# Kernel tuning notes

Measured on AMD Instinct MI355X. Metric: run time of the kernel, lower is better.

Reference implementation:

```python
import jax, jax.numpy as jnp
import numpy as np

N = 50000      # nodes
E = 800000     # edges
D = 128        # h_dim
R = 8          # num_rel
B = 4          # num_bases (< R -> basis decomposition)
L = 2          # num_conv
BN_EPS = 1e-3  # keras BatchNormalization default epsilon


def setup_inputs() -> dict:
    key = jax.random.key(0)
    ks = jax.random.split(key, 10)
    node_feat = jax.random.normal(ks[0], (N, D), dtype=jnp.float32)
    src = jax.random.randint(ks[1], (E,), 0, N)
    dst = jax.random.randint(ks[2], (E,), 0, N)
    etype = jax.random.randint(ks[3], (E,), 0, R)
    s = 1.0 / np.sqrt(D)
    W_emb = jax.random.normal(ks[4], (D, D), dtype=jnp.float32) * s
    b_emb = jnp.zeros((D,), dtype=jnp.float32)
    bases = jax.random.normal(ks[5], (L, B, D, D), dtype=jnp.float32) * s
    w_coe = jax.random.normal(ks[6], (L, R, B), dtype=jnp.float32) * 0.3
    self_loop = jax.random.normal(ks[7], (L, D, D), dtype=jnp.float32) * s
    bn_gamma = jnp.ones((L, D), dtype=jnp.float32)
    bn_beta = jnp.zeros((L, D), dtype=jnp.float32)
    bn_mean = jnp.zeros((L, D), dtype=jnp.float32)
    bn_var = jnp.ones((L, D), dtype=jnp.float32)
    return {"node_feat": node_feat, "W_emb": W_emb, "b_emb": b_emb,
            "bases": bases, "w_coe": w_coe, "self_loop": self_loop,
            "bn_gamma": bn_gamma, "bn_beta": bn_beta,
            "bn_mean": bn_mean, "bn_var": bn_var,
            "src": src, "dst": dst, "etype": etype}


def _edge_norm(etype, dst, dtype):
    # compute_norm: per edge type r, node_norm[dst] = 1/(#edges of type r into dst),
    # later types overwrite earlier ones (tensor_scatter_nd_update in the loop).
    node_norm = jnp.zeros((N,), dtype=dtype)
    for r in range(R):  # unique edge types, fixed ascending order
        mask = (etype == r).astype(dtype)
        cnt = jax.ops.segment_sum(mask, dst, num_segments=N)
        node_norm = jnp.where(cnt > 0, 1.0 / jnp.maximum(cnt, 1.0), node_norm)
    return node_norm[dst][:, None]  # [E, 1], norm of each edge's destination


def reference(node_feat, W_emb, b_emb, bases, w_coe, self_loop,
              bn_gamma, bn_beta, bn_mean, bn_var, src, dst, etype):
    # embedding Dense
    h = node_feat @ W_emb + b_emb                     # [N, D]
    norm = _edge_norm(etype, dst, h.dtype)            # [E, 1]
    for l in range(L):
        # basis decomposition: W[r] = sum_b w_coe[r,b] * bases[b]
        W = jnp.einsum('rb,bdf->rdf', w_coe[l], bases[l])   # [R, D, D]
        # transform all nodes under every relation, then gather per edge
        # (same math as per-type boolean_mask + matmul in low_mem path)
        T = jnp.einsum('nd,rdf->rnf', h, W)                 # [R, N, D]
        msg = T[etype, src] * norm                          # [E, D]
        agg = jax.ops.segment_sum(msg, dst, num_segments=N) # sum reduce -> [N, D]
        h = agg + h @ self_loop[l]
        # BatchNormalization, inference mode (training=None)
        h = bn_gamma[l] * (h - bn_mean[l]) * jax.lax.rsqrt(bn_var[l] + BN_EPS) + bn_beta[l]
        h = jax.nn.relu(h)
        # Dropout is identity at inference
    return h
```

## Files before the change

### kernel.cpp

```cpp
#include <hip/hip_runtime.h>

#define Dh 128
#define NN 50000
#define EE 800000
#define RR 8
#define BB 4
#define LL 2
#define KTOT 640
#define KA0 512
#define BN_EPS 1e-3f
#define NR (NN * RR)
#define NBLK 196

#define N8    (NN * Dh / 8)
#define BT_N  (LL * Dh * KTOT)
#define WE_N  (Dh * Dh)
#define EPI_N (3 * Dh)
#define Z4_N  (NR / 4)
#define PREP_TOT (N8 + BT_N + WE_N + EPI_N + Z4_N)

typedef __attribute__((ext_vector_type(8))) short bf16x8;
typedef __attribute__((ext_vector_type(4))) float f32x4;

__device__ inline unsigned short f2bf(float x) {
    unsigned u = __float_as_uint(x);
    unsigned r = (u + 0x7fffu + ((u >> 16) & 1u)) >> 16;
    return (unsigned short)r;
}

__global__ __launch_bounds__(256) void prep_kernel(
    const float* __restrict__ nf, const float* __restrict__ bases,
    const float* __restrict__ self_loop, const float* __restrict__ W_emb,
    const float* __restrict__ b_emb,
    const float* __restrict__ bn_gamma, const float* __restrict__ bn_beta,
    const float* __restrict__ bn_mean, const float* __restrict__ bn_var,
    unsigned short* __restrict__ nf_bf, unsigned short* __restrict__ BT,
    unsigned short* __restrict__ WembT,
    float* __restrict__ sc, float* __restrict__ sh, int* __restrict__ counts)
{
    int idx = blockIdx.x * 256 + threadIdx.x;
    if (idx < N8) {
        size_t base = (size_t)idx * 8;
        float4 v0 = *(const float4*)&nf[base];
        float4 v1 = *(const float4*)&nf[base + 4];
        unsigned short o[8] = { f2bf(v0.x), f2bf(v0.y), f2bf(v0.z), f2bf(v0.w),
                                f2bf(v1.x), f2bf(v1.y), f2bf(v1.z), f2bf(v1.w) };
        *(uint4*)&nf_bf[base] = *(uint4*)o;
        return;
    }
    idx -= N8;
    if (idx < BT_N) {
        int l = idx / (Dh * KTOT);
        int rem = idx - l * (Dh * KTOT);
        int f = rem / KTOT;
        int k = rem - f * KTOT;
        float v;
        if (k < KA0) v = bases[(((l * BB + (k >> 7)) * Dh) + (k & 127)) * Dh + f];
        else         v = self_loop[((size_t)l * Dh + (k - KA0)) * Dh + f];
        BT[(size_t)(l * Dh + f) * KTOT + k] = f2bf(v);
        return;
    }
    idx -= BT_N;
    if (idx < WE_N) {
        int f = idx >> 7, d = idx & 127;
        WembT[f * Dh + d] = f2bf(W_emb[d * Dh + f]);
        return;
    }
    idx -= WE_N;
    if (idx < EPI_N) {
        int cfg = idx >> 7, d = idx & 127;
        float s, t;
        if (cfg == 0) { s = 1.f; t = b_emb[d]; }
        else {
            int l = cfg - 1;
            float sv = bn_gamma[l * Dh + d] * rsqrtf(bn_var[l * Dh + d] + BN_EPS);
            s = sv;
            t = bn_beta[l * Dh + d] - bn_mean[l * Dh + d] * sv;
        }
        sc[cfg * Dh + d] = s; sh[cfg * Dh + d] = t;
        return;
    }
    idx -= EPI_N;
    if (idx < Z4_N) ((int4*)counts)[idx] = make_int4(0, 0, 0, 0);
}

__global__ __launch_bounds__(256) void gemm_bn_kernel(
    const unsigned short* __restrict__ A0, int ka0,
    const unsigned short* __restrict__ A1,
    const unsigned short* __restrict__ BT, int K,
    const float* __restrict__ sc, const float* __restrict__ sh,
    void* __restrict__ outp, int out_fp32, int do_relu, int M)
{
    __shared__ unsigned short a_s[128][72];
    __shared__ unsigned short b_s[128][72];
    int t = threadIdx.x;
    int wave = t >> 6, lane = t & 63;
    int wr = wave * 32;
    int n16 = lane & 15, quad = lane >> 4;
    int row0 = blockIdx.x * 128;

    f32x4 acc[2][8];
    #pragma unroll
    for (int i = 0; i < 2; i++)
        #pragma unroll
        for (int j = 0; j < 8; j++)
            acc[i][j] = (f32x4){0.f, 0.f, 0.f, 0.f};

    int nchunk = K >> 6;
    for (int ch = 0; ch < nchunk; ch++) {
        int k0 = ch * 64;
        {
            int srow = t >> 1, seg = t & 1;
            int gr = row0 + srow;
            int kk = k0 + seg * 32;
            const uint4* gp;
            if (kk < ka0) gp = (const uint4*)&A0[(size_t)gr * ka0 + kk];
            else          gp = (const uint4*)&A1[(size_t)gr * Dh + (kk - ka0)];
            #pragma unroll
            for (int i = 0; i < 4; i++) {
                uint4 v = make_uint4(0u, 0u, 0u, 0u);
                if (gr < M) v = gp[i];
                *(uint4*)&a_s[srow][seg * 32 + i * 8] = v;
            }
        }
        {
            int f = t >> 1, seg = t & 1;
            const uint4* bp = (const uint4*)&BT[(size_t)f * K + k0 + seg * 32];
            #pragma unroll
            for (int i = 0; i < 4; i++)
                *(uint4*)&b_s[f][seg * 32 + i * 8] = bp[i];
        }
        __syncthreads();
        #pragma unroll
        for (int ks = 0; ks < 2; ks++) {
            bf16x8 af[2], bfr[8];
            #pragma unroll
            for (int i = 0; i < 2; i++)
                af[i] = *(const bf16x8*)&a_s[wr + i * 16 + n16][ks * 32 + quad * 8];
            #pragma unroll
            for (int j = 0; j < 8; j++)
                bfr[j] = *(const bf16x8*)&b_s[j * 16 + n16][ks * 32 + quad * 8];
            #pragma unroll
            for (int i = 0; i < 2; i++)
                #pragma unroll
                for (int j = 0; j < 8; j++)
                    acc[i][j] = __builtin_amdgcn_mfma_f32_16x16x32_bf16(
                        af[i], bfr[j], acc[i][j], 0, 0, 0);
        }
        __syncthreads();
    }

    float sj[8], tj[8];
    #pragma unroll
    for (int j = 0; j < 8; j++) {
        int col = j * 16 + n16;
        sj[j] = sc[col]; tj[j] = sh[col];
    }
    #pragma unroll
    for (int i = 0; i < 2; i++) {
        #pragma unroll
        for (int v = 0; v < 4; v++) {
            int gr = row0 + wr + i * 16 + quad * 4 + v;
            if (gr < M) {
                #pragma unroll
                for (int j = 0; j < 8; j++) {
                    float y = acc[i][j][v] * sj[j] + tj[j];
                    if (do_relu) y = fmaxf(y, 0.f);
                    int col = j * 16 + n16;
                    if (out_fp32) ((float*)outp)[(size_t)gr * Dh + col] = y;
                    else ((unsigned short*)outp)[(size_t)gr * Dh + col] = f2bf(y);
                }
            }
        }
    }
}

__global__ __launch_bounds__(256) void count_kernel(
    const int* __restrict__ dst, const int* __restrict__ etype,
    int* __restrict__ counts)
{
    int idx = blockIdx.x * 256 + threadIdx.x;
    if (idx >= EE / 4) return;
    int4 d = ((const int4*)dst)[idx];
    int4 t = ((const int4*)etype)[idx];
    atomicAdd(&counts[d.x * RR + t.x], 1);
    atomicAdd(&counts[d.y * RR + t.y], 1);
    atomicAdd(&counts[d.z * RR + t.z], 1);
    atomicAdd(&counts[d.w * RR + t.w], 1);
}

__global__ __launch_bounds__(256) void norm_scan1_kernel(
    const int* __restrict__ counts, float* __restrict__ node_norm,
    int* __restrict__ row_ptr, int* __restrict__ bsum)
{
    __shared__ int s[256];
    int t = threadIdx.x;
    int n = blockIdx.x * 256 + t;
    int total = 0; float norm = 0.f;
    if (n < NN) {
        #pragma unroll
        for (int r = 0; r < RR; r++) {
            int c = counts[n * RR + r];
            total += c;
            if (c > 0) norm = 1.0f / (float)c;
        }
        node_norm[n] = norm;
    }
    s[t] = total;
    __syncthreads();
    #pragma unroll
    for (int off = 1; off < 256; off <<= 1) {
        int v = (t >= off) ? s[t - off] : 0;
        __syncthreads();
        s[t] += v;
        __syncthreads();
    }
    if (n < NN) row_ptr[n] = s[t] - total;
    if (t == 255) bsum[blockIdx.x] = s[255];
}

__global__ __launch_bounds__(256) void scan2_kernel(
    const int* __restrict__ bsum, int* __restrict__ boffset)
{
    __shared__ int s[256];
    int t = threadIdx.x;
    int d = (t < NBLK) ? bsum[t] : 0;
    s[t] = d;
    __syncthreads();
    #pragma unroll
    for (int off = 1; off < 256; off <<= 1) {
        int v = (t >= off) ? s[t - off] : 0;
        __syncthreads();
        s[t] += v;
        __syncthreads();
    }
    if (t <= NBLK) boffset[t] = s[t] - d;
}

__global__ __launch_bounds__(256) void scan3_kernel(
    int* __restrict__ row_ptr, int* __restrict__ cursor,
    const int* __restrict__ boffset)
{
    int t = threadIdx.x;
    int n = blockIdx.x * 256 + t;
    if (n < NN) {
        int v = row_ptr[n] + boffset[blockIdx.x];
        row_ptr[n] = v;
        cursor[n]  = v;
    }
    if (blockIdx.x == 0 && t == 0) row_ptr[NN] = EE;
}

__global__ __launch_bounds__(256) void fill_kernel(
    const int* __restrict__ src, const int* __restrict__ dst,
    const int* __restrict__ etype, int* __restrict__ cursor,
    unsigned* __restrict__ packed)
{
    int idx = blockIdx.x * 256 + threadIdx.x;
    if (idx >= EE / 4) return;
    int4 d  = ((const int4*)dst)[idx];
    int4 sr = ((const int4*)src)[idx];
    int4 et = ((const int4*)etype)[idx];
    int p0 = atomicAdd(&cursor[d.x], 1);
    int p1 = atomicAdd(&cursor[d.y], 1);
    int p2 = atomicAdd(&cursor[d.z], 1);
    int p3 = atomicAdd(&cursor[d.w], 1);
    packed[p0] = (unsigned)sr.x | ((unsigned)et.x << 16);
    packed[p1] = (unsigned)sr.y | ((unsigned)et.y << 16);
    packed[p2] = (unsigned)sr.z | ((unsigned)et.z << 16);
    packed[p3] = (unsigned)sr.w | ((unsigned)et.w << 16);
}

__global__ __launch_bounds__(256) void agg_basis_kernel(
    const unsigned* __restrict__ h32, const int* __restrict__ row_ptr,
    const unsigned* __restrict__ packed, const float* __restrict__ node_norm,
    const float* __restrict__ wco,
    unsigned* __restrict__ aggB)
{
    __shared__ float4 co_s[RR];
    int t = threadIdx.x;
    if (t < RR) co_s[t] = ((const float4*)wco)[t];
    __syncthreads();
    int wave = t >> 6, lane = t & 63;
    int n = blockIdx.x * 4 + wave;
    if (n >= NN) return;
    int s = row_ptr[n];
    int e = row_ptr[n + 1];
    float a0[BB], a1[BB];
    #pragma unroll
    for (int b = 0; b < BB; b++) { a0[b] = 0.f; a1[b] = 0.f; }
    int i = s;
    for (; i + 8 <= e; i += 8) {
        unsigned p[8], hv[8];
        #pragma unroll
        for (int k = 0; k < 8; k++) p[k] = packed[i + k];
        #pragma unroll
        for (int k = 0; k < 8; k++)
            hv[k] = h32[(size_t)(p[k] & 0xffffu) * 64 + lane];
        #pragma unroll
        for (int k = 0; k < 8; k++) {
            float4 co = co_s[p[k] >> 16];
            float lo = __uint_as_float(hv[k] << 16);
            float hi = __uint_as_float(hv[k] & 0xffff0000u);
            a0[0] += co.x * lo; a1[0] += co.x * hi;
            a0[1] += co.y * lo; a1[1] += co.y * hi;
            a0[2] += co.z * lo; a1[2] += co.z * hi;
            a0[3] += co.w * lo; a1[3] += co.w * hi;
        }
    }
    if (i < e) {
        unsigned p[8], hv[8];
        #pragma unroll
        for (int k = 0; k < 8; k++) {
            int j = i + k;
            p[k] = packed[j < e ? j : (e - 1)];
        }
        #pragma unroll
        for (int k = 0; k < 8; k++)
            hv[k] = h32[(size_t)(p[k] & 0xffffu) * 64 + lane];
        #pragma unroll
        for (int k = 0; k < 8; k++) {
            float vm = (i + k < e) ? 1.f : 0.f;
            float4 co = co_s[p[k] >> 16];
            float lo = __uint_as_float(hv[k] << 16) * vm;
            float hi = __uint_as_float(hv[k] & 0xffff0000u) * vm;
            a0[0] += co.x * lo; a1[0] += co.x * hi;
            a0[1] += co.y * lo; a1[1] += co.y * hi;
            a0[2] += co.z * lo; a1[2] += co.z * hi;
            a0[3] += co.w * lo; a1[3] += co.w * hi;
        }
    }
    float norm = node_norm[n];
    #pragma unroll
    for (int b = 0; b < BB; b++) {
        unsigned o = (unsigned)f2bf(a0[b] * norm) |
                     ((unsigned)f2bf(a1[b] * norm) << 16);
        aggB[(size_t)n * 256 + b * 64 + lane] = o;
    }
}

extern "C" void kernel_launch(void* const* d_in, const int* in_sizes, int n_in,
                              void* d_out, int out_size, void* d_ws, size_t ws_size,
                              hipStream_t stream)
{
    const float* node_feat = (const float*)d_in[0];
    const float* W_emb     = (const float*)d_in[1];
    const float* b_emb     = (const float*)d_in[2];
    const float* bases     = (const float*)d_in[3];
    const float* w_coe     = (const float*)d_in[4];
    const float* self_loop = (const float*)d_in[5];
    const float* bn_gamma  = (const float*)d_in[6];
    const float* bn_beta   = (const float*)d_in[7];
    const float* bn_mean   = (const float*)d_in[8];
    const float* bn_var    = (const float*)d_in[9];
    const int*   src       = (const int*)d_in[10];
    const int*   dst       = (const int*)d_in[11];
    const int*   etype     = (const int*)d_in[12];

    char* ws = (char*)d_ws;
    size_t off = 0;
    unsigned short* h0 = (unsigned short*)(ws + off);     off += (size_t)NN * Dh * 2;
    unsigned short* h1 = (unsigned short*)(ws + off);     off += (size_t)NN * Dh * 2;
    unsigned short* nf_bf = (unsigned short*)(ws + off);  off += (size_t)NN * Dh * 2;
    unsigned short* aggB = (unsigned short*)(ws + off);   off += (size_t)NN * KA0 * 2;
    unsigned short* BT = (unsigned short*)(ws + off);     off += (size_t)LL * Dh * KTOT * 2;
    unsigned short* WembT = (unsigned short*)(ws + off);  off += (size_t)Dh * Dh * 2;
    float* sc = (float*)(ws + off);                       off += 3 * Dh * 4;
    float* sh = (float*)(ws + off);                       off += 3 * Dh * 4;
    float* node_norm = (float*)(ws + off);                off += (size_t)NN * 4;
    int* counts = (int*)(ws + off);                       off += (size_t)NR * 4;
    int* row_ptr = (int*)(ws + off);                      off += ((size_t)NN + 4) * 4;
    int* cursor = (int*)(ws + off);                       off += (size_t)NN * 4;
    int* bsum = (int*)(ws + off);                         off += 256 * 4;
    int* boffset = (int*)(ws + off);                      off += 260 * 4;
    unsigned* packed = (unsigned*)(ws + off);             off += (size_t)EE * 4;

    const int e4_blocks = (EE / 4 + 255) / 256;
    const int node_blocks = (NN + 255) / 256;
    const int prep_blocks = (PREP_TOT + 255) / 256;
    const int gemm_blocks = (NN + 127) / 128;
    const int agg_blocks = (NN + 3) / 4;

    prep_kernel<<<prep_blocks, 256, 0, stream>>>(
        node_feat, bases, self_loop, W_emb, b_emb,
        bn_gamma, bn_beta, bn_mean, bn_var,
        nf_bf, BT, WembT, sc, sh, counts);

    count_kernel<<<e4_blocks, 256, 0, stream>>>(dst, etype, counts);
    norm_scan1_kernel<<<node_blocks, 256, 0, stream>>>(counts, node_norm, row_ptr, bsum);
    scan2_kernel<<<1, 256, 0, stream>>>(bsum, boffset);
    scan3_kernel<<<node_blocks, 256, 0, stream>>>(row_ptr, cursor, boffset);
    fill_kernel<<<e4_blocks, 256, 0, stream>>>(src, dst, etype, cursor, packed);

    gemm_bn_kernel<<<gemm_blocks, 256, 0, stream>>>(
        nf_bf, Dh, nullptr, WembT, Dh, sc, sh, h0, 0, 0, NN);

    agg_basis_kernel<<<agg_blocks, 256, 0, stream>>>(
        (const unsigned*)h0, row_ptr, packed, node_norm, w_coe, (unsigned*)aggB);
    gemm_bn_kernel<<<gemm_blocks, 256, 0, stream>>>(
        aggB, KA0, h0, BT, KTOT, sc + Dh, sh + Dh, h1, 0, 1, NN);

    agg_basis_kernel<<<agg_blocks, 256, 0, stream>>>(
        (const unsigned*)h1, row_ptr, packed, node_norm, w_coe + RR * BB, (unsigned*)aggB);
    gemm_bn_kernel<<<gemm_blocks, 256, 0, stream>>>(
        aggB, KA0, h1, BT + Dh * KTOT, KTOT, sc + 2 * Dh, sh + 2 * Dh, d_out, 1, 1, NN);
}
```

Measured before the change: 325.8 us.

## Shrink GEMM tile to 64 rows with register double-buffered loads; tweak fill and gather

The GEMM tile drops from 128 to 64 rows per block, which doubles the block count, and the loop now prefetches the next K-chunk into registers while the current chunk is computed. This aims to raise occupancy and hide global load latency, at the cost of reloading the B tile twice as often. The fill kernel now handles 2 edges per thread instead of 4, giving more threads for the atomics. The aggregation kernel reads packed edge indices through readfirstlane so they stay scalar, and uses 32-bit address arithmetic.

```diff
diff --git a/kernel.cpp b/kernel.cpp
--- a/kernel.cpp
+++ b/kernel.cpp
@@ -91,63 +91,80 @@
     const float* __restrict__ sc, const float* __restrict__ sh,
     void* __restrict__ outp, int out_fp32, int do_relu, int M)
 {
-    __shared__ unsigned short a_s[128][72];
+    __shared__ unsigned short a_s[64][72];
     __shared__ unsigned short b_s[128][72];
     int t = threadIdx.x;
     int wave = t >> 6, lane = t & 63;
-    int wr = wave * 32;
     int n16 = lane & 15, quad = lane >> 4;
-    int row0 = blockIdx.x * 128;
-
-    f32x4 acc[2][8];
-    #pragma unroll
-    for (int i = 0; i < 2; i++)
-        #pragma unroll
-        for (int j = 0; j < 8; j++)
-            acc[i][j] = (f32x4){0.f, 0.f, 0.f, 0.f};
+    int row0 = blockIdx.x * 64;
+
+    int arow = t >> 2, aseg = t & 3;
+    int brow = t >> 1, bseg = t & 1;
+
+    f32x4 acc[8];
+    #pragma unroll
+    for (int j = 0; j < 8; j++) acc[j] = (f32x4){0.f, 0.f, 0.f, 0.f};
 
     int nchunk = K >> 6;
-    for (int ch = 0; ch < nchunk; ch++) {
-        int k0 = ch * 64;
-        {
-            int srow = t >> 1, seg = t & 1;
-            int gr = row0 + srow;
-            int kk = k0 + seg * 32;
-            const uint4* gp;
-            if (kk < ka0) gp = (const uint4*)&A0[(size_t)gr * ka0 + kk];
-            else          gp = (const uint4*)&A1[(size_t)gr * Dh + (kk - ka0)];
-            #pragma unroll
-            for (int i = 0; i < 4; i++) {
-                uint4 v = make_uint4(0u, 0u, 0u, 0u);
-                if (gr < M) v = gp[i];
-                *(uint4*)&a_s[srow][seg * 32 + i * 8] = v;
-            }
-        }
-        {
-            int f = t >> 1, seg = t & 1;
-            const uint4* bp = (const uint4*)&BT[(size_t)f * K + k0 + seg * 32];
-            #pragma unroll
-            for (int i = 0; i < 4; i++)
-                *(uint4*)&b_s[f][seg * 32 + i * 8] = bp[i];
-        }
-        __syncthreads();
+
+    uint4 arA[2], brA[4], arB[2], brB[4];
+
+    auto LOADC = [&](int k0, uint4* ar, uint4* br) {
+        int gr = row0 + arow;
+        int kk = k0 + aseg * 16;
+        const uint4* gp;
+        if (kk < ka0) gp = (const uint4*)&A0[(size_t)gr * ka0 + kk];
+        else          gp = (const uint4*)&A1[(size_t)gr * Dh + (kk - ka0)];
+        #pragma unroll
+        for (int i = 0; i < 2; i++) {
+            uint4 v = make_uint4(0u, 0u, 0u, 0u);
+            if (gr < M) v = gp[i];
+            ar[i] = v;
+        }
+        const uint4* bp = (const uint4*)&BT[(size_t)brow * K + k0 + bseg * 32];
+        #pragma unroll
+        for (int i = 0; i < 4; i++) br[i] = bp[i];
+    };
+    auto STOREC = [&](const uint4* ar, const uint4* br) {
+        #pragma unroll
+        for (int i = 0; i < 2; i++)
+            *(uint4*)&a_s[arow][aseg * 16 + i * 8] = ar[i];
+        #pragma unroll
+        for (int i = 0; i < 4; i++)
+            *(uint4*)&b_s[brow][bseg * 32 + i * 8] = br[i];
+    };
+    auto COMPUTE = [&]() {
         #pragma unroll
         for (int ks = 0; ks < 2; ks++) {
-            bf16x8 af[2], bfr[8];
-            #pragma unroll
-            for (int i = 0; i < 2; i++)
-                af[i] = *(const bf16x8*)&a_s[wr + i * 16 + n16][ks * 32 + quad * 8];
+            bf16x8 af, bfr[8];
+            af = *(const bf16x8*)&a_s[wave * 16 + n16][ks * 32 + quad * 8];
             #pragma unroll
             for (int j = 0; j < 8; j++)
                 bfr[j] = *(const bf16x8*)&b_s[j * 16 + n16][ks * 32 + quad * 8];
             #pragma unroll
-            for (int i = 0; i < 2; i++)
-                #pragma unroll
-                for (int j = 0; j < 8; j++)
-                    acc[i][j] = __builtin_amdgcn_mfma_f32_16x16x32_bf16(
-                        af[i], bfr[j], acc[i][j], 0, 0, 0);
-        }
-        __syncthreads();
+            for (int j = 0; j < 8; j++)
+                acc[j] = __builtin_amdgcn_mfma_f32_16x16x32_bf16(
+                    af, bfr[j], acc[j], 0, 0, 0);
+        }
+    };
+
+    LOADC(0, arA, brA);
+    int ch = 0;
+    while (true) {
+        STOREC(arA, brA);
+        __syncthreads();
+        if (ch + 1 < nchunk) LOADC((ch + 1) * 64, arB, brB);
+        COMPUTE();
+        __syncthreads();
+        ch++;
+        if (ch >= nchunk) break;
+        STOREC(arB, brB);
+        __syncthreads();
+        if (ch + 1 < nchunk) LOADC((ch + 1) * 64, arA, brA);
+        COMPUTE();
+        __syncthreads();
+        ch++;
+        if (ch >= nchunk) break;
     }
 
     float sj[8], tj[8];
@@ -157,19 +174,16 @@
         sj[j] = sc[col]; tj[j] = sh[col];
     }
     #pragma unroll
-    for (int i = 0; i < 2; i++) {
-        #pragma unroll
-        for (int v = 0; v < 4; v++) {
-            int gr = row0 + wr + i * 16 + quad * 4 + v;
-            if (gr < M) {
-                #pragma unroll
-                for (int j = 0; j < 8; j++) {
-                    float y = acc[i][j][v] * sj[j] + tj[j];
-                    if (do_relu) y = fmaxf(y, 0.f);
-                    int col = j * 16 + n16;
-                    if (out_fp32) ((float*)outp)[(size_t)gr * Dh + col] = y;
-                    else ((unsigned short*)outp)[(size_t)gr * Dh + col] = f2bf(y);
-                }
+    for (int v = 0; v < 4; v++) {
+        int gr = row0 + wave * 16 + quad * 4 + v;
+        if (gr < M) {
+            #pragma unroll
+            for (int j = 0; j < 8; j++) {
+                float y = acc[j][v] * sj[j] + tj[j];
+                if (do_relu) y = fmaxf(y, 0.f);
+                int col = j * 16 + n16;
+                if (out_fp32) ((float*)outp)[(size_t)gr * Dh + col] = y;
+                else ((unsigned short*)outp)[(size_t)gr * Dh + col] = f2bf(y);
             }
         }
     }
@@ -257,18 +271,14 @@
     unsigned* __restrict__ packed)
 {
     int idx = blockIdx.x * 256 + threadIdx.x;
-    if (idx >= EE / 4) return;
-    int4 d  = ((const int4*)dst)[idx];
-    int4 sr = ((const int4*)src)[idx];
-    int4 et = ((const int4*)etype)[idx];
+    if (idx >= EE / 2) return;
+    int2 d  = ((const int2*)dst)[idx];
+    int2 sr = ((const int2*)src)[idx];
+    int2 et = ((const int2*)etype)[idx];
     int p0 = atomicAdd(&cursor[d.x], 1);
     int p1 = atomicAdd(&cursor[d.y], 1);
-    int p2 = atomicAdd(&cursor[d.z], 1);
-    int p3 = atomicAdd(&cursor[d.w], 1);
     packed[p0] = (unsigned)sr.x | ((unsigned)et.x << 16);
     packed[p1] = (unsigned)sr.y | ((unsigned)et.y << 16);
-    packed[p2] = (unsigned)sr.z | ((unsigned)et.z << 16);
-    packed[p3] = (unsigned)sr.w | ((unsigned)et.w << 16);
 }
 
 __global__ __launch_bounds__(256) void agg_basis_kernel(
@@ -293,10 +303,11 @@
     for (; i + 8 <= e; i += 8) {
         unsigned p[8], hv[8];
         #pragma unroll
-        for (int k = 0; k < 8; k++) p[k] = packed[i + k];
-        #pragma unroll
         for (int k = 0; k < 8; k++)
-            hv[k] = h32[(size_t)(p[k] & 0xffffu) * 64 + lane];
+            p[k] = (unsigned)__builtin_amdgcn_readfirstlane((int)packed[i + k]);
+        #pragma unroll
+        for (int k = 0; k < 8; k++)
+            hv[k] = h32[((p[k] & 0xffffu) << 6) + (unsigned)lane];
         #pragma unroll
         for (int k = 0; k < 8; k++) {
             float4 co = co_s[p[k] >> 16];
@@ -313,11 +324,12 @@
         #pragma unroll
         for (int k = 0; k < 8; k++) {
             int j = i + k;
-            p[k] = packed[j < e ? j : (e - 1)];
+            p[k] = (unsigned)__builtin_amdgcn_readfirstlane(
+                (int)packed[j < e ? j : (e - 1)]);
         }
         #pragma unroll
         for (int k = 0; k < 8; k++)
-            hv[k] = h32[(size_t)(p[k] & 0xffffu) * 64 + lane];
+            hv[k] = h32[((p[k] & 0xffffu) << 6) + (unsigned)lane];
         #pragma unroll
         for (int k = 0; k < 8; k++) {
             float vm = (i + k < e) ? 1.f : 0.f;
@@ -376,9 +388,10 @@
     unsigned* packed = (unsigned*)(ws + off);             off += (size_t)EE * 4;
 
     const int e4_blocks = (EE / 4 + 255) / 256;
+    const int e2_blocks = (EE / 2 + 255) / 256;
     const int node_blocks = (NN + 255) / 256;
     const int prep_blocks = (PREP_TOT + 255) / 256;
-    const int gemm_blocks = (NN + 127) / 128;
+    const int gemm_blocks = (NN + 63) / 64;
     const int agg_blocks = (NN + 3) / 4;
 
     prep_kernel<<<prep_blocks, 256, 0, stream>>>(
@@ -390,7 +403,7 @@
     norm_scan1_kernel<<<node_blocks, 256, 0, stream>>>(counts, node_norm, row_ptr, bsum);
     scan2_kernel<<<1, 256, 0, stream>>>(bsum, boffset);
     scan3_kernel<<<node_blocks, 256, 0, stream>>>(row_ptr, cursor, boffset);
-    fill_kernel<<<e4_blocks, 256, 0, stream>>>(src, dst, etype, cursor, packed);
+    fill_kernel<<<e2_blocks, 256, 0, stream>>>(src, dst, etype, cursor, packed);
 
     gemm_bn_kernel<<<gemm_blocks, 256, 0, stream>>>(
         nf_bf, Dh, nullptr, WembT, Dh, sc, sh, h0, 0, 0, NN);
```

Measured after the change: 413.8 us. 27.0% more time.
